# Kernel tuning notes

Measured on AMD Instinct MI355X. Metric: run time of the kernel, lower is better.

The kernel has to match this reference:

```python
import math
import jax, jax.numpy as jnp
import numpy as np

D_MODEL = 1024
NUM_HEADS = 16
D_K = D_MODEL // NUM_HEADS
RANK = 16
B, L = 2, 2048


def setup_inputs() -> dict:
    key = jax.random.key(0)
    ks = jax.random.split(key, 10)
    w_scale = 0.02  # keep activations well-scaled like trained linears
    return {
        "x_q": jax.random.normal(ks[0], (B, L, D_MODEL), jnp.float32),
        "x_kv": jax.random.normal(ks[1], (B, L, D_MODEL), jnp.float32),
        "Wq": jax.random.normal(ks[2], (D_MODEL, D_MODEL), jnp.float32) * w_scale,
        "bq": jnp.zeros((D_MODEL,), jnp.float32),
        "Wk": jax.random.normal(ks[3], (D_MODEL, D_MODEL), jnp.float32) * w_scale,
        "bk": jnp.zeros((D_MODEL,), jnp.float32),
        "Wv": jax.random.normal(ks[4], (D_MODEL, D_MODEL), jnp.float32) * w_scale,
        "bv": jnp.zeros((D_MODEL,), jnp.float32),
        "Wo": jax.random.normal(ks[5], (D_MODEL, D_MODEL), jnp.float32) * w_scale,
        "bo": jnp.zeros((D_MODEL,), jnp.float32),
        "U_bil": jax.random.normal(ks[6], (NUM_HEADS, D_K, RANK), jnp.float32) * 0.02,
        "V_bil": jax.random.normal(ks[7], (NUM_HEADS, D_K, RANK), jnp.float32) * 0.02,
        "padding_mask": jnp.zeros((B, L), bool),  # True = padded KV position
    }


def reference(x_q, x_kv, Wq, bq, Wk, bk, Wv, bv, Wo, bo, U_bil, V_bil, padding_mask):
    b, l, _ = x_q.shape
    # torch nn.Linear: y = x @ W.T + b
    Q = (x_q @ Wq.T + bq).reshape(b, l, NUM_HEADS, D_K).transpose(0, 2, 1, 3)  # [B,H,L,dk]
    K = (x_kv @ Wk.T + bk).reshape(b, l, NUM_HEADS, D_K).transpose(0, 2, 1, 3)
    V = (x_kv @ Wv.T + bv).reshape(b, l, NUM_HEADS, D_K).transpose(0, 2, 1, 3)
    # low-rank bilinear projections: [B,H,L,rank]
    Q_proj = jnp.einsum("bhld,hdr->bhlr", Q, U_bil)
    K_proj = jnp.einsum("bhld,hdr->bhlr", K, V_bil)
    scores = jnp.einsum("bhqr,bhkr->bhqk", Q_proj, K_proj) / math.sqrt(RANK)  # [B,H,L,L]
    scores = jnp.where(padding_mask[:, None, None, :], jnp.float32(-10000.0), scores)
    attn = jax.nn.softmax(scores, axis=-1)  # dropout is identity in eval mode
    ctx = jnp.einsum("bhqk,bhkd->bhqd", attn, V)
    ctx = ctx.transpose(0, 2, 1, 3).reshape(b, l, D_MODEL)
    return ctx @ Wo.T + bo
```

## Files before the change

kernel.cpp:

```cpp
#include <hip/hip_runtime.h>
#include <hip/hip_bf16.h>

#define DM   1024
#define NH   16
#define DK   64
#define RK   16
#define BB   2
#define LL   2048
#define TT   (BB*LL)
#define NSPL 2


typedef float f4   __attribute__((ext_vector_type(4)));
typedef float f16v __attribute__((ext_vector_type(16)));
typedef short s8v  __attribute__((ext_vector_type(8)));
typedef unsigned int u2v __attribute__((ext_vector_type(2)));
typedef unsigned int u4v __attribute__((ext_vector_type(4)));

static __device__ __forceinline__ unsigned short f2b(float f) {
  __hip_bfloat16 h = __float2bfloat16(f);
  unsigned short u;
  __builtin_memcpy(&u, &h, 2);
  return u;
}
static __device__ __forceinline__ float b2f(unsigned short u) {
  __hip_bfloat16 h;
  __builtin_memcpy(&h, &u, 2);
  return __bfloat162float(h);
}

static __device__ __forceinline__ void gld_lds16(const void* g, void* l) {
  __builtin_amdgcn_global_load_lds(
      (const __attribute__((address_space(1))) unsigned int*)g,
      (__attribute__((address_space(3))) unsigned int*)l, 16, 0, 0);
}

static __device__ __forceinline__ void cast_rng(
    const float* __restrict__ s, unsigned short* __restrict__ d,
    int n4, int lb, int nb, int tid) {
  for (int i = lb*256 + tid; i < n4; i += nb*256) {
    const float4 v = ((const float4*)s)[i];
    ushort4 o;
    o.x = f2b(v.x); o.y = f2b(v.y); o.z = f2b(v.z); o.w = f2b(v.w);
    ((ushort4*)d)[i] = o;
  }
}

__global__ __launch_bounds__(256) void prep_k(
    const float* __restrict__ xq,  const float* __restrict__ xkv,
    const float* __restrict__ Wv,  const float* __restrict__ Wo,
    unsigned short* __restrict__ xq_b,  unsigned short* __restrict__ xkv_b,
    unsigned short* __restrict__ Wv_b,  unsigned short* __restrict__ Wo_b,
    const float* __restrict__ Wq,  const float* __restrict__ Wk,
    const float* __restrict__ Uq,  const float* __restrict__ Uk,
    unsigned short* __restrict__ Aq, unsigned short* __restrict__ Ak,
    const float* __restrict__ bq,  const float* __restrict__ bk,
    float* __restrict__ bpq, float* __restrict__ bpk) {
  __shared__ float sh[64*16 + 4*64];
  const int x = blockIdx.x, tid = threadIdx.x;
  if (x < 1024) {
    cast_rng(xq,  xq_b,  TT*DM/4, x,        1024, tid);
  } else if (x < 2048) {
    cast_rng(xkv, xkv_b, TT*DM/4, x - 1024, 1024, tid);
  } else if (x < 2304) {
    cast_rng(Wv,  Wv_b,  DM*DM/4, x - 2048, 256, tid);
  } else if (x < 2560) {
    cast_rng(Wo,  Wo_b,  DM*DM/4, x - 2304, 256, tid);
  } else if (x < 3072) {
    const int fidx = x - 2560;
    const int sel = fidx >> 8, f = fidx & 255;
    const float* W = sel ? Wk : Wq;
    const float* U = sel ? Uk : Uq;
    unsigned short* At = sel ? Ak : Aq;
    const int i0 = (f & 15) * 64, h = f >> 4;
    float* Us = sh;
    float* Ws = sh + 1024;
    const int il = tid & 63, rr = tid >> 6;
    for (int t = tid; t < 64*16; t += 256)
      Us[t] = U[(size_t)(h*DK + (t >> 4))*RK + (t & 15)];
    float acc[4] = {};
    for (int d0 = 0; d0 < DK; d0 += 4) {
      __syncthreads();
      Ws[rr*64 + il] = W[(size_t)(h*DK + d0 + rr)*DM + i0 + il];
      __syncthreads();
#pragma unroll
      for (int dd = 0; dd < 4; ++dd) {
        const float w = Ws[dd*64 + il];
#pragma unroll
        for (int j = 0; j < 4; ++j)
          acc[j] += w * Us[(d0 + dd)*16 + rr*4 + j];
      }
    }
#pragma unroll
    for (int j = 0; j < 4; ++j)
      At[(size_t)(h*RK + rr*4 + j)*DM + i0 + il] = f2b(acc[j]);
  } else {
    const int h = tid >> 4, r = tid & 15;
    float aq = 0.f, ak = 0.f;
    for (int d = 0; d < DK; ++d) {
      aq += bq[h*DK + d] * Uq[(size_t)(h*DK + d)*RK + r];
      ak += bk[h*DK + d] * Uk[(size_t)(h*DK + d)*RK + r];
    }
    bpq[tid] = aq; bpk[tid] = ak;
  }
}

__global__ __launch_bounds__(256) void proj_k(
    const unsigned short* __restrict__ xq_b, const unsigned short* __restrict__ xkv_b,
    const unsigned short* __restrict__ Atq,  const unsigned short* __restrict__ Atk,
    const float* __restrict__ bpq, const float* __restrict__ bpk,
    unsigned short* __restrict__ Qp, unsigned short* __restrict__ Kp,
    const unsigned short* __restrict__ Wv_b, const float* __restrict__ bv,
    unsigned short* __restrict__ Vt) {
  __shared__ __align__(16) unsigned short shm[8192];
  const int f = blockIdx.x, tid = threadIdx.x;
  const int wave = tid >> 6, lane = tid & 63;
  const int quad = lane >> 4, l15 = lane & 15;
  const int ar = tid >> 2, ac = (tid & 3) * 8;
  const f4 z = {0.f, 0.f, 0.f, 0.f};

  if (f < 256) {
    const int xb = f & 63, yb = (f >> 6) & 1, zb = f >> 7;
    const unsigned short* Ag = zb ? xkv_b : xq_b;
    const unsigned short* Bg = zb ? Atk : Atq;
    const float* bias = zb ? bpk : bpq;
    unsigned short* C = zb ? Kp : Qp;
    unsigned short* Xs = shm;
    unsigned short* Bs = shm + 2048;
    const int t0 = xb*64, n0 = yb*128, nh = wave*32;
    f4 acc[4][2];
#pragma unroll
    for (int a = 0; a < 4; ++a) { acc[a][0] = z; acc[a][1] = z; }
    for (int k0 = 0; k0 < DM; k0 += 32) {
      __syncthreads();
      gld_lds16(&Ag[(size_t)(t0 + ar)*DM + k0 + ac],      &Xs[wave*512]);
      gld_lds16(&Bg[(size_t)(n0 + ar)*DM + k0 + ac],      &Bs[wave*512]);
      gld_lds16(&Bg[(size_t)(n0 + 64 + ar)*DM + k0 + ac], &Bs[2048 + wave*512]);
      __syncthreads();
      s8v af[4], bf[2];
#pragma unroll
      for (int ms = 0; ms < 4; ++ms)
        af[ms] = *(const s8v*)&Xs[(ms*16 + l15)*32 + quad*8];
#pragma unroll
      for (int ns = 0; ns < 2; ++ns)
        bf[ns] = *(const s8v*)&Bs[(nh + ns*16 + l15)*32 + quad*8];
#pragma unroll
      for (int ms = 0; ms < 4; ++ms)
#pragma unroll
        for (int ns = 0; ns < 2; ++ns)
          acc[ms][ns] = __builtin_amdgcn_mfma_f32_16x16x32_bf16(
              af[ms], bf[ns], acc[ms][ns], 0, 0, 0);
    }
#pragma unroll
    for (int ms = 0; ms < 4; ++ms) {
      const int tb = t0 + ms*16 + quad*4;
#pragma unroll
      for (int ns = 0; ns < 2; ++ns) {
        const int o = n0 + nh + ns*16 + l15;
        const float bvv = bias[o];
        f4 a = acc[ms][ns];
#pragma unroll
        for (int rg = 0; rg < 4; ++rg) {
          const int tt = tb + rg;
          C[(((size_t)(tt >> 11)*NH + (o >> 4))*LL + (tt & 2047))*RK + (o & 15)]
              = f2b(a[rg] + bvv);
        }
      }
    }
  } else {
    const int g = f - 256, gx = g & 31, gy = g >> 5;
    unsigned short* As = shm;
    unsigned short* Bs = shm + 4096;
    const int t0 = gx*128, n0 = gy*128;
    f4 acc[2][8];
#pragma unroll
    for (int m = 0; m < 2; ++m)
#pragma unroll
      for (int n = 0; n < 8; ++n) acc[m][n] = z;
    for (int k0 = 0; k0 < DM; k0 += 32) {
      __syncthreads();
      gld_lds16(&xkv_b[(size_t)(t0 + ar)*DM + k0 + ac],      &As[wave*512]);
      gld_lds16(&xkv_b[(size_t)(t0 + 64 + ar)*DM + k0 + ac], &As[2048 + wave*512]);
      gld_lds16(&Wv_b[(size_t)(n0 + ar)*DM + k0 + ac],       &Bs[wave*512]);
      gld_lds16(&Wv_b[(size_t)(n0 + 64 + ar)*DM + k0 + ac],  &Bs[2048 + wave*512]);
      __syncthreads();
      s8v af[2], bf[8];
#pragma unroll
      for (int ms = 0; ms < 2; ++ms)
        af[ms] = *(const s8v*)&As[(wave*32 + ms*16 + l15)*32 + quad*8];
#pragma unroll
      for (int ns = 0; ns < 8; ++ns)
        bf[ns] = *(const s8v*)&Bs[(ns*16 + l15)*32 + quad*8];
#pragma unroll
      for (int ms = 0; ms < 2; ++ms)
#pragma unroll
        for (int ns = 0; ns < 8; ++ns)
          acc[ms][ns] = __builtin_amdgcn_mfma_f32_16x16x32_bf16(
              af[ms], bf[ns], acc[ms][ns], 0, 0, 0);
    }
#pragma unroll
    for (int ms = 0; ms < 2; ++ms) {
      const int tb = t0 + wave*32 + ms*16 + quad*4;
#pragma unroll
      for (int ns = 0; ns < 8; ++ns) {
        const int o = n0 + ns*16 + l15;
        const float bvv = bv[o];
        f4 a = acc[ms][ns];
        const int bb = tb >> 11, l = tb & 2047;
        ushort4 pk;
        pk.x = f2b(a[0] + bvv); pk.y = f2b(a[1] + bvv);
        pk.z = f2b(a[2] + bvv); pk.w = f2b(a[3] + bvv);
        *(ushort4*)&Vt[((size_t)bb*DM + o)*LL + l] = pk;
      }
    }
  }
}

template<bool MASKED>
static __device__ __forceinline__ void softmax_pack(
    const f16v& s0, const f16v& s1, const unsigned long long mb, const int hi,
    float& den, unsigned int (&Pd)[2][4][2]) {
#pragma unroll
  for (int nt = 0; nt < 2; ++nt) {
    const f16v& sv = nt ? s1 : s0;
#pragma unroll
    for (int r = 0; r < 4; ++r) {
      float ep[4];
#pragma unroll
      for (int j = 0; j < 4; ++j) {
        float em = __expf(sv[r*4 + j] * 0.25f);
        if (MASKED) {
          const int kloc = nt*32 + j + 8*r + 4*hi;
          if ((mb >> kloc) & 1ull) em = 0.f;
        }
        den += em;
        ep[j] = em - 1.f;
      }
      asm("v_cvt_pk_bf16_f32 %0, %1, %2"
          : "=v"(Pd[nt][r][0]) : "v"(ep[0]), "v"(ep[1]));
      asm("v_cvt_pk_bf16_f32 %0, %1, %2"
          : "=v"(Pd[nt][r][1]) : "v"(ep[2]), "v"(ep[3]));
    }
  }
}

__global__ __launch_bounds__(256) void attn_k(
    const unsigned short* __restrict__ Qp, const unsigned short* __restrict__ Kp,
    const unsigned short* __restrict__ Vt,
    const unsigned char* __restrict__ msk,
    unsigned short* __restrict__ P, float* __restrict__ denP,
    float* __restrict__ Vsum) {
  __shared__ __align__(16) unsigned short Ks[2][2][64][8];
  __shared__ __align__(16) unsigned short Vs[2][8][64][8];
  const int tid = threadIdx.x;

  if (blockIdx.z == 4) {
    if (blockIdx.y >= BB) return;
    const int h = blockIdx.x, b = blockIdx.y;
    const int d = tid >> 2, part = tid & 3;
    const unsigned short* row = Vt + ((size_t)b*DM + h*DK + d)*LL + part*512;
    float s = 0.f;
    for (int i = 0; i < 512; i += 8) {
      const s8v v = *(const s8v*)&row[i];
#pragma unroll
      for (int j = 0; j < 8; ++j) s += b2f((unsigned short)v[j]);
    }
    s += __shfl_xor(s, 1);
    s += __shfl_xor(s, 2);
    if (part == 0) Vsum[((size_t)b*NH + h)*DK + d] = s;
    return;
  }

  const int q0 = blockIdx.x * 128, h = blockIdx.y;
  const int b = blockIdx.z & (BB - 1), ksp = blockIdx.z >> 1;
  const int kbeg = ksp * (LL / NSPL);
  const int NT = (LL / NSPL) / 64;
  const int w = tid >> 6, lane = tid & 63;
  const int l31 = lane & 31, hi = lane >> 5;

  const s8v qfrag = *(const s8v*)&Qp[
      (((size_t)b*NH + h)*LL + q0 + w*32 + l31)*RK + hi*8];

  const int sr = tid >> 2, sp = tid & 3;
  const unsigned short* __restrict__ Vrow =
      Vt + ((size_t)b*DM + h*DK + sr)*LL + kbeg;
  const unsigned short* __restrict__ Kbase =
      Kp + (((size_t)b*NH + h)*LL + kbeg + sr)*RK + sp*4;
  const unsigned char*  __restrict__ Mrow = msk + (size_t)b*LL + kbeg + lane;

  u2v kpre; s8v vpre0, vpre1;
  unsigned char mcur, mnext;

  kpre  = *(const u2v*)&Kbase[0];
  vpre0 = *(const s8v*)&Vrow[sp*16];
  vpre1 = *(const s8v*)&Vrow[sp*16 + 8];
  mcur  = Mrow[0];
  *(u2v*)&Ks[0][sp>>1][sr][(sp&1)*4] = kpre;
  *(s8v*)&Vs[0][sp*2][sr][0]   = vpre0;
  *(s8v*)&Vs[0][sp*2+1][sr][0] = vpre1;
  kpre  = *(const u2v*)&Kbase[(size_t)64*RK];
  vpre0 = *(const s8v*)&Vrow[64 + sp*16];
  vpre1 = *(const s8v*)&Vrow[64 + sp*16 + 8];
  mnext = Mrow[64];
  __syncthreads();

  f16v acc0, acc1, z16;
#pragma unroll
  for (int i = 0; i < 16; ++i) { acc0[i] = 0.f; acc1[i] = 0.f; z16[i] = 0.f; }
  float den = 0.f;

  for (int t = 0; t < NT; ++t) {
    const int cur = t & 1;
    const unsigned long long mb = __ballot(mcur != 0);

    const s8v kf0 = *(const s8v*)&Ks[cur][hi][l31][0];
    const s8v kf1 = *(const s8v*)&Ks[cur][hi][32 + l31][0];

    const f16v s0 = __builtin_amdgcn_mfma_f32_32x32x16_bf16(kf0, qfrag, z16, 0, 0, 0);
    const f16v s1 = __builtin_amdgcn_mfma_f32_32x32x16_bf16(kf1, qfrag, z16, 0, 0, 0);

    unsigned int Pd[2][4][2];
    if (__builtin_expect(mb != 0ull, 0))
      softmax_pack<true >(s0, s1, mb, hi, den, Pd);
    else
      softmax_pack<false>(s0, s1, mb, hi, den, Pd);

#pragma unroll
    for (int kc = 0; kc < 4; ++kc) {
      const int nt = kc >> 1, a = (kc & 1)*2;
      const u2v r0 = __builtin_amdgcn_permlane32_swap(
          Pd[nt][a][0], Pd[nt][a+1][0], false, false);
      const u2v r1 = __builtin_amdgcn_permlane32_swap(
          Pd[nt][a][1], Pd[nt][a+1][1], false, false);
      u4v efi;
      efi[0] = r0[0];
      efi[1] = r1[0];
      efi[2] = r0[1];
      efi[3] = r1[1];
      const s8v ef = __builtin_bit_cast(s8v, efi);
      const s8v vf0 = *(const s8v*)&Vs[cur][kc*2 + hi][l31][0];
      const s8v vf1 = *(const s8v*)&Vs[cur][kc*2 + hi][32 + l31][0];
      acc0 = __builtin_amdgcn_mfma_f32_32x32x16_bf16(ef, vf0, acc0, 0, 0, 0);
      acc1 = __builtin_amdgcn_mfma_f32_32x32x16_bf16(ef, vf1, acc1, 0, 0, 0);
    }

    if (t + 1 < NT) {
      *(u2v*)&Ks[cur^1][sp>>1][sr][(sp&1)*4] = kpre;
      *(s8v*)&Vs[cur^1][sp*2][sr][0]   = vpre0;
      *(s8v*)&Vs[cur^1][sp*2+1][sr][0] = vpre1;
      const int tn = (t + 2 < NT) ? t + 2 : NT - 1;
      kpre  = *(const u2v*)&Kbase[(size_t)tn*64*RK];
      vpre0 = *(const s8v*)&Vrow[tn*64 + sp*16];
      vpre1 = *(const s8v*)&Vrow[tn*64 + sp*16 + 8];
      mcur  = mnext;
      mnext = Mrow[tn*64];
    }
    __syncthreads();
  }

  den += __shfl_xor(den, 32);
  if (hi == 0)
    denP[(((size_t)ksp*BB + b)*NH + h)*LL + q0 + w*32 + l31] = den;

#pragma unroll
  for (int rg = 0; rg < 16; ++rg) {
    const int qr = (rg & 3) + 8*(rg >> 2) + 4*hi;
    const size_t pbase =
        ((size_t)ksp*TT + b*LL + q0 + w*32 + qr)*DM + h*DK;
    P[pbase + l31]      = f2b(acc0[rg]);
    P[pbase + 32 + l31] = f2b(acc1[rg]);
  }
}

__global__ __launch_bounds__(256) void outred_k(
    const unsigned short* __restrict__ P, const float* __restrict__ Vsum,
    const float* __restrict__ denP, const unsigned short* __restrict__ Bg,
    const float* __restrict__ bias, float* __restrict__ C) {
  __shared__ __align__(16) unsigned short Xs[64*32];
  __shared__ __align__(16) unsigned short Bs[128*32];
  const int f = blockIdx.x;
  const int t0 = (f & 63) * 64, n0 = (f >> 6) * 128;
  const int tid = threadIdx.x, wave = tid >> 6, lane = tid & 63;
  const int quad = lane >> 4, l15 = lane & 15;
  const int nh = wave * 32;
  const int ar = tid >> 2, ac = (tid & 3) * 8;
  const int trow = t0 + ar;
  const int b = trow >> 11, l = trow & 2047;
  const unsigned short* __restrict__ P0 = P + (size_t)trow*DM;
  const unsigned short* __restrict__ P1 = P + ((size_t)TT + trow)*DM;
  const float* __restrict__ vsb = Vsum + (size_t)b*DM;
  const float* __restrict__ dp0 = denP + ((size_t)b*NH)*LL + l;
  const float* __restrict__ dp1 = denP + (((size_t)BB + b)*NH)*LL + l;

  const f4 z = {0.f, 0.f, 0.f, 0.f};
  f4 acc[4][2];
#pragma unroll
  for (int a = 0; a < 4; ++a) { acc[a][0] = z; acc[a][1] = z; }

  for (int k0 = 0; k0 < DM; k0 += 32) {
    __syncthreads();
    gld_lds16(&Bg[(size_t)(n0 + ar)*DM + k0 + ac],      &Bs[wave*512]);
    gld_lds16(&Bg[(size_t)(n0 + 64 + ar)*DM + k0 + ac], &Bs[2048 + wave*512]);
    const int hk = k0 >> 6;
    const float dn = dp0[(size_t)hk*LL] + dp1[(size_t)hk*LL];
    const float inv = 1.f / fmaxf(dn, 1e-30f);
    const s8v p0 = *(const s8v*)&P0[k0 + ac];
    const s8v p1 = *(const s8v*)&P1[k0 + ac];
    const f4 vs0 = *(const f4*)&vsb[k0 + ac];
    const f4 vs1 = *(const f4*)&vsb[k0 + ac + 4];
    s8v av;
#pragma unroll
    for (int j = 0; j < 4; ++j) {
      const float c0 = (vs0[j] + b2f((unsigned short)p0[j])
                               + b2f((unsigned short)p1[j])) * inv;
      const float c1 = (vs1[j] + b2f((unsigned short)p0[4+j])
                               + b2f((unsigned short)p1[4+j])) * inv;
      av[j]     = (short)f2b(c0);
      av[4 + j] = (short)f2b(c1);
    }
    *(s8v*)&Xs[ar*32 + ac] = av;
    __syncthreads();

    s8v af[4], bf[2];
#pragma unroll
    for (int ms = 0; ms < 4; ++ms)
      af[ms] = *(const s8v*)&Xs[(ms*16 + l15)*32 + quad*8];
#pragma unroll
    for (int ns = 0; ns < 2; ++ns)
      bf[ns] = *(const s8v*)&Bs[(nh + ns*16 + l15)*32 + quad*8];
#pragma unroll
    for (int ms = 0; ms < 4; ++ms)
#pragma unroll
      for (int ns = 0; ns < 2; ++ns)
        acc[ms][ns] = __builtin_amdgcn_mfma_f32_16x16x32_bf16(
            af[ms], bf[ns], acc[ms][ns], 0, 0, 0);
  }

#pragma unroll
  for (int ms = 0; ms < 4; ++ms) {
    const int tb = t0 + ms*16 + quad*4;
#pragma unroll
    for (int ns = 0; ns < 2; ++ns) {
      const int o = n0 + nh + ns*16 + l15;
      const float bv = bias[o];
      f4 a = acc[ms][ns];
#pragma unroll
      for (int rg = 0; rg < 4; ++rg)
        C[(size_t)(tb + rg)*DM + o] = a[rg] + bv;
    }
  }
}

extern "C" void kernel_launch(void* const* d_in, const int* in_sizes, int n_in,
                              void* d_out, int out_size, void* d_ws, size_t ws_size,
                              hipStream_t stream) {
  (void)in_sizes; (void)n_in; (void)out_size; (void)ws_size;
  const float* x_q   = (const float*)d_in[0];
  const float* x_kv  = (const float*)d_in[1];
  const float* Wq    = (const float*)d_in[2];
  const float* bq    = (const float*)d_in[3];
  const float* Wk    = (const float*)d_in[4];
  const float* bk    = (const float*)d_in[5];
  const float* Wv    = (const float*)d_in[6];
  const float* bv    = (const float*)d_in[7];
  const float* Wo    = (const float*)d_in[8];
  const float* bo    = (const float*)d_in[9];
  const float* U_bil = (const float*)d_in[10];
  const float* V_bil = (const float*)d_in[11];
  const unsigned char* pmask = (const unsigned char*)d_in[12];
  float* out = (float*)d_out;

  char* w = (char*)d_ws;
  unsigned short* xq_b  = (unsigned short*)(w);
  unsigned short* xkv_b = (unsigned short*)(w +  8388608);
  unsigned short* Wv_b  = (unsigned short*)(w + 16777216);
  unsigned short* Wo_b  = (unsigned short*)(w + 18874368);
  unsigned short* Atq   = (unsigned short*)(w + 20971520);
  unsigned short* Atk   = (unsigned short*)(w + 21495808);
  float*          bpq   = (float*)(w + 22020096);
  float*          bpk   = (float*)(w + 22021120);
  unsigned short* Qp    = (unsigned short*)(w + 22022144);
  unsigned short* Kp    = (unsigned short*)(w + 24119296);
  unsigned short* Vt    = (unsigned short*)(w + 26216448);
  float*          Vsum  = (float*)(w + 34605056);
  float*          denP  = (float*)(w + 34613248);
  unsigned short* Pbuf  = (unsigned short*)w;

  prep_k<<<3073, 256, 0, stream>>>(
      x_q, x_kv, Wv, Wo, xq_b, xkv_b, Wv_b, Wo_b,
      Wq, Wk, U_bil, V_bil, Atq, Atk, bq, bk, bpq, bpk);
  proj_k<<<512, 256, 0, stream>>>(
      xq_b, xkv_b, Atq, Atk, bpq, bpk, Qp, Kp, Wv_b, bv, Vt);
  attn_k<<<dim3(LL/128, NH, 5), 256, 0, stream>>>(
      Qp, Kp, Vt, pmask, Pbuf, denP, Vsum);
  outred_k<<<512, 256, 0, stream>>>(Pbuf, Vsum, denP, Wo_b, bo, out);
}
```

Measured before the change: 226.1 us.

## Double-buffer LDS staging in projection and output GEMMs, restructure output combine

```diff
diff --git a/kernel.cpp b/kernel.cpp
--- a/kernel.cpp
+++ b/kernel.cpp
@@ -33,6 +33,11 @@
   __builtin_amdgcn_global_load_lds(
       (const __attribute__((address_space(1))) unsigned int*)g,
       (__attribute__((address_space(3))) unsigned int*)l, 16, 0, 0);
+}
+
+static __device__ __forceinline__ void wait_vm0_barrier() {
+  asm volatile("s_waitcnt vmcnt(0)" ::: "memory");
+  __builtin_amdgcn_s_barrier();
 }
 
 static __device__ __forceinline__ void cast_rng(
@@ -112,7 +117,7 @@
     unsigned short* __restrict__ Qp, unsigned short* __restrict__ Kp,
     const unsigned short* __restrict__ Wv_b, const float* __restrict__ bv,
     unsigned short* __restrict__ Vt) {
-  __shared__ __align__(16) unsigned short shm[8192];
+  __shared__ __align__(16) unsigned short shm[16384];
   const int f = blockIdx.x, tid = threadIdx.x;
   const int wave = tid >> 6, lane = tid & 63;
   const int quad = lane >> 4, l15 = lane & 15;
@@ -126,30 +131,37 @@
     const float* bias = zb ? bpk : bpq;
     unsigned short* C = zb ? Kp : Qp;
     unsigned short* Xs = shm;
-    unsigned short* Bs = shm + 2048;
+    unsigned short* Bq = shm + 4096;
     const int t0 = xb*64, n0 = yb*128, nh = wave*32;
     f4 acc[4][2];
 #pragma unroll
     for (int a = 0; a < 4; ++a) { acc[a][0] = z; acc[a][1] = z; }
+
+    auto STAGE = [&](int buf, int k0) {
+      gld_lds16(&Ag[(size_t)(t0 + ar)*DM + k0 + ac],      &Xs[buf*2048 + wave*512]);
+      gld_lds16(&Bg[(size_t)(n0 + ar)*DM + k0 + ac],      &Bq[buf*4096 + wave*512]);
+      gld_lds16(&Bg[(size_t)(n0 + 64 + ar)*DM + k0 + ac], &Bq[buf*4096 + 2048 + wave*512]);
+    };
+    STAGE(0, 0);
+    wait_vm0_barrier();
+    int cur = 0;
     for (int k0 = 0; k0 < DM; k0 += 32) {
-      __syncthreads();
-      gld_lds16(&Ag[(size_t)(t0 + ar)*DM + k0 + ac],      &Xs[wave*512]);
-      gld_lds16(&Bg[(size_t)(n0 + ar)*DM + k0 + ac],      &Bs[wave*512]);
-      gld_lds16(&Bg[(size_t)(n0 + 64 + ar)*DM + k0 + ac], &Bs[2048 + wave*512]);
-      __syncthreads();
+      if (k0 + 32 < DM) STAGE(cur ^ 1, k0 + 32);
       s8v af[4], bf[2];
 #pragma unroll
       for (int ms = 0; ms < 4; ++ms)
-        af[ms] = *(const s8v*)&Xs[(ms*16 + l15)*32 + quad*8];
+        af[ms] = *(const s8v*)&Xs[cur*2048 + (ms*16 + l15)*32 + quad*8];
 #pragma unroll
       for (int ns = 0; ns < 2; ++ns)
-        bf[ns] = *(const s8v*)&Bs[(nh + ns*16 + l15)*32 + quad*8];
+        bf[ns] = *(const s8v*)&Bq[cur*4096 + (nh + ns*16 + l15)*32 + quad*8];
 #pragma unroll
       for (int ms = 0; ms < 4; ++ms)
 #pragma unroll
         for (int ns = 0; ns < 2; ++ns)
           acc[ms][ns] = __builtin_amdgcn_mfma_f32_16x16x32_bf16(
               af[ms], bf[ns], acc[ms][ns], 0, 0, 0);
+      wait_vm0_barrier();
+      cur ^= 1;
     }
 #pragma unroll
     for (int ms = 0; ms < 4; ++ms) {
@@ -170,33 +182,40 @@
   } else {
     const int g = f - 256, gx = g & 31, gy = g >> 5;
     unsigned short* As = shm;
-    unsigned short* Bs = shm + 4096;
+    unsigned short* Bs = shm + 8192;
     const int t0 = gx*128, n0 = gy*128;
     f4 acc[2][8];
 #pragma unroll
     for (int m = 0; m < 2; ++m)
 #pragma unroll
       for (int n = 0; n < 8; ++n) acc[m][n] = z;
+
+    auto STAGE = [&](int buf, int k0) {
+      gld_lds16(&xkv_b[(size_t)(t0 + ar)*DM + k0 + ac],      &As[buf*4096 + wave*512]);
+      gld_lds16(&xkv_b[(size_t)(t0 + 64 + ar)*DM + k0 + ac], &As[buf*4096 + 2048 + wave*512]);
+      gld_lds16(&Wv_b[(size_t)(n0 + ar)*DM + k0 + ac],       &Bs[buf*4096 + wave*512]);
+      gld_lds16(&Wv_b[(size_t)(n0 + 64 + ar)*DM + k0 + ac],  &Bs[buf*4096 + 2048 + wave*512]);
+    };
+    STAGE(0, 0);
+    wait_vm0_barrier();
+    int cur = 0;
     for (int k0 = 0; k0 < DM; k0 += 32) {
-      __syncthreads();
-      gld_lds16(&xkv_b[(size_t)(t0 + ar)*DM + k0 + ac],      &As[wave*512]);
-      gld_lds16(&xkv_b[(size_t)(t0 + 64 + ar)*DM + k0 + ac], &As[2048 + wave*512]);
-      gld_lds16(&Wv_b[(size_t)(n0 + ar)*DM + k0 + ac],       &Bs[wave*512]);
-      gld_lds16(&Wv_b[(size_t)(n0 + 64 + ar)*DM + k0 + ac],  &Bs[2048 + wave*512]);
-      __syncthreads();
+      if (k0 + 32 < DM) STAGE(cur ^ 1, k0 + 32);
       s8v af[2], bf[8];
 #pragma unroll
       for (int ms = 0; ms < 2; ++ms)
-        af[ms] = *(const s8v*)&As[(wave*32 + ms*16 + l15)*32 + quad*8];
+        af[ms] = *(const s8v*)&As[cur*4096 + (wave*32 + ms*16 + l15)*32 + quad*8];
 #pragma unroll
       for (int ns = 0; ns < 8; ++ns)
-        bf[ns] = *(const s8v*)&Bs[(ns*16 + l15)*32 + quad*8];
+        bf[ns] = *(const s8v*)&Bs[cur*4096 + (ns*16 + l15)*32 + quad*8];
 #pragma unroll
       for (int ms = 0; ms < 2; ++ms)
 #pragma unroll
         for (int ns = 0; ns < 8; ++ns)
           acc[ms][ns] = __builtin_amdgcn_mfma_f32_16x16x32_bf16(
               af[ms], bf[ns], acc[ms][ns], 0, 0, 0);
+      wait_vm0_barrier();
+      cur ^= 1;
     }
 #pragma unroll
     for (int ms = 0; ms < 2; ++ms) {
@@ -376,8 +395,11 @@
     const unsigned short* __restrict__ P, const float* __restrict__ Vsum,
     const float* __restrict__ denP, const unsigned short* __restrict__ Bg,
     const float* __restrict__ bias, float* __restrict__ C) {
-  __shared__ __align__(16) unsigned short Xs[64*32];
-  __shared__ __align__(16) unsigned short Bs[128*32];
+  __shared__ __align__(16) unsigned short P0s[2][2048];
+  __shared__ __align__(16) unsigned short P1s[2][2048];
+  __shared__ __align__(16) unsigned short Bs[2][4096];
+  __shared__ float vsS[1024];
+  __shared__ float invS[64][16];
   const int f = blockIdx.x;
   const int t0 = (f & 63) * 64, n0 = (f >> 6) * 128;
   const int tid = threadIdx.x, wave = tid >> 6, lane = tid & 63;
@@ -385,55 +407,77 @@
   const int nh = wave * 32;
   const int ar = tid >> 2, ac = (tid & 3) * 8;
   const int trow = t0 + ar;
-  const int b = trow >> 11, l = trow & 2047;
-  const unsigned short* __restrict__ P0 = P + (size_t)trow*DM;
-  const unsigned short* __restrict__ P1 = P + ((size_t)TT + trow)*DM;
-  const float* __restrict__ vsb = Vsum + (size_t)b*DM;
-  const float* __restrict__ dp0 = denP + ((size_t)b*NH)*LL + l;
-  const float* __restrict__ dp1 = denP + (((size_t)BB + b)*NH)*LL + l;
+  const int b = t0 >> 11;
+
+  for (int i = tid; i < 1024; i += 256)
+    vsS[i] = Vsum[(size_t)b*DM + i];
+  {
+    const int r = tid >> 2, h0 = (tid & 3) * 4;
+    const int lr = (t0 + r) & 2047;
+#pragma unroll
+    for (int j = 0; j < 4; ++j) {
+      const int h = h0 + j;
+      const float dn = denP[((size_t)b*NH + h)*LL + lr] +
+                       denP[(((size_t)BB + b)*NH + h)*LL + lr];
+      invS[r][h] = 1.f / fmaxf(dn, 1e-30f);
+    }
+  }
+
+  auto STAGE = [&](int buf, int k0) {
+    gld_lds16(&P[(size_t)trow*DM + k0 + ac],             &P0s[buf][wave*512]);
+    gld_lds16(&P[((size_t)TT + trow)*DM + k0 + ac],      &P1s[buf][wave*512]);
+    gld_lds16(&Bg[(size_t)(n0 + ar)*DM + k0 + ac],       &Bs[buf][wave*512]);
+    gld_lds16(&Bg[(size_t)(n0 + 64 + ar)*DM + k0 + ac],  &Bs[buf][2048 + wave*512]);
+  };
+  STAGE(0, 0);
+  asm volatile("s_waitcnt vmcnt(0) lgkmcnt(0)" ::: "memory");
+  __builtin_amdgcn_s_barrier();
 
   const f4 z = {0.f, 0.f, 0.f, 0.f};
   f4 acc[4][2];
 #pragma unroll
   for (int a = 0; a < 4; ++a) { acc[a][0] = z; acc[a][1] = z; }
 
+  int cur = 0;
   for (int k0 = 0; k0 < DM; k0 += 32) {
-    __syncthreads();
-    gld_lds16(&Bg[(size_t)(n0 + ar)*DM + k0 + ac],      &Bs[wave*512]);
-    gld_lds16(&Bg[(size_t)(n0 + 64 + ar)*DM + k0 + ac], &Bs[2048 + wave*512]);
+    if (k0 + 32 < DM) STAGE(cur ^ 1, k0 + 32);
     const int hk = k0 >> 6;
-    const float dn = dp0[(size_t)hk*LL] + dp1[(size_t)hk*LL];
-    const float inv = 1.f / fmaxf(dn, 1e-30f);
-    const s8v p0 = *(const s8v*)&P0[k0 + ac];
-    const s8v p1 = *(const s8v*)&P1[k0 + ac];
-    const f4 vs0 = *(const f4*)&vsb[k0 + ac];
-    const f4 vs1 = *(const f4*)&vsb[k0 + ac + 4];
-    s8v av;
-#pragma unroll
-    for (int j = 0; j < 4; ++j) {
-      const float c0 = (vs0[j] + b2f((unsigned short)p0[j])
-                               + b2f((unsigned short)p1[j])) * inv;
-      const float c1 = (vs1[j] + b2f((unsigned short)p0[4+j])
-                               + b2f((unsigned short)p1[4+j])) * inv;
-      av[j]     = (short)f2b(c0);
-      av[4 + j] = (short)f2b(c1);
-    }
-    *(s8v*)&Xs[ar*32 + ac] = av;
-    __syncthreads();
-
+    const f4 vq0 = *(const f4*)&vsS[k0 + quad*8];
+    const f4 vq1 = *(const f4*)&vsS[k0 + quad*8 + 4];
     s8v af[4], bf[2];
 #pragma unroll
-    for (int ms = 0; ms < 4; ++ms)
-      af[ms] = *(const s8v*)&Xs[(ms*16 + l15)*32 + quad*8];
+    for (int ms = 0; ms < 4; ++ms) {
+      const int r16 = ms*16 + l15;
+      const float inv = invS[r16][hk];
+      const s8v p0 = *(const s8v*)&P0s[cur][r16*32 + quad*8];
+      const s8v p1 = *(const s8v*)&P1s[cur][r16*32 + quad*8];
+      float e[8];
+#pragma unroll
+      for (int j = 0; j < 4; ++j) {
+        e[j]     = (vq0[j] + b2f((unsigned short)p0[j])
+                           + b2f((unsigned short)p1[j])) * inv;
+        e[4 + j] = (vq1[j] + b2f((unsigned short)p0[4+j])
+                           + b2f((unsigned short)p1[4+j])) * inv;
+      }
+      unsigned int d0, d1, d2, d3;
+      asm("v_cvt_pk_bf16_f32 %0, %1, %2" : "=v"(d0) : "v"(e[0]), "v"(e[1]));
+      asm("v_cvt_pk_bf16_f32 %0, %1, %2" : "=v"(d1) : "v"(e[2]), "v"(e[3]));
+      asm("v_cvt_pk_bf16_f32 %0, %1, %2" : "=v"(d2) : "v"(e[4]), "v"(e[5]));
+      asm("v_cvt_pk_bf16_f32 %0, %1, %2" : "=v"(d3) : "v"(e[6]), "v"(e[7]));
+      u4v efi; efi[0] = d0; efi[1] = d1; efi[2] = d2; efi[3] = d3;
+      af[ms] = __builtin_bit_cast(s8v, efi);
+    }
 #pragma unroll
     for (int ns = 0; ns < 2; ++ns)
-      bf[ns] = *(const s8v*)&Bs[(nh + ns*16 + l15)*32 + quad*8];
+      bf[ns] = *(const s8v*)&Bs[cur][(nh + ns*16 + l15)*32 + quad*8];
 #pragma unroll
     for (int ms = 0; ms < 4; ++ms)
 #pragma unroll
       for (int ns = 0; ns < 2; ++ns)
         acc[ms][ns] = __builtin_amdgcn_mfma_f32_16x16x32_bf16(
             af[ms], bf[ns], acc[ms][ns], 0, 0, 0);
+    wait_vm0_barrier();
+    cur ^= 1;
   }
 
 #pragma unroll
```

Result: no change. 229.4 us (+1.5%).
